# Kernel tuning notes

Hardware: AMD Instinct MI355X
Metric: run time of the kernel (lower is better)

The kernel has to match this reference:

```python
import jax, jax.numpy as jnp
import numpy as np

B, K, D, DS = 32, 64, 4, 4
H = 512            # hidden_dim
HH = H // 2        # hidden_hidden_dim = 256
NA = 2             # n_action


def _lin(k, out_d, in_d):
    kw, kb = jax.random.split(k)
    w = jax.random.normal(kw, (out_d, in_d), dtype=jnp.float32) * (in_d ** -0.5)
    b = jax.random.normal(kb, (out_d,), dtype=jnp.float32) * 0.01
    return w, b


def setup_inputs() -> dict:
    key = jax.random.key(0)
    ks = jax.random.split(key, 16)
    state = jax.random.normal(ks[0], (B, DS), dtype=jnp.float32)
    obs = jax.random.normal(ks[1], (B, D, K), dtype=jnp.float32)
    layer_w, layer_b = _lin(ks[2], H, DS)
    e1_w, e1_b = _lin(ks[3], H, 2 * D)
    e2_w, e2_b = _lin(ks[4], H, H)
    e3_w, e3_b = _lin(ks[5], H, H)
    ln_g = jnp.ones((H,), jnp.float32)
    ln_b = jnp.zeros((H,), jnp.float32)
    n1_w, n1_b = _lin(ks[6], H, D + H + DS)
    n2_w, n2_b = _lin(ks[7], HH, H)
    mu1_w, mu1_b = _lin(ks[8], 256, H + H)
    mu2_w, mu2_b = _lin(ks[9], 128, 256)
    mu3_w, mu3_b = _lin(ks[10], NA, 128)
    s1_w, s1_b = _lin(ks[11], 256, H + H)
    s2_w, s2_b = _lin(ks[12], 128, 256)
    s3_w, s3_b = _lin(ks[13], NA, 128)
    return dict(state=state, obs=obs, layer_w=layer_w, layer_b=layer_b,
                e1_w=e1_w, e1_b=e1_b, e2_w=e2_w, e2_b=e2_b, e3_w=e3_w, e3_b=e3_b,
                ln_g=ln_g, ln_b=ln_b, n1_w=n1_w, n1_b=n1_b, n2_w=n2_w, n2_b=n2_b,
                mu1_w=mu1_w, mu1_b=mu1_b, mu2_w=mu2_w, mu2_b=mu2_b, mu3_w=mu3_w, mu3_b=mu3_b,
                s1_w=s1_w, s1_b=s1_b, s2_w=s2_w, s2_b=s2_b, s3_w=s3_w, s3_b=s3_b)


def _dense(x, w, b):
    return x @ w.T + b


def reference(state, obs, layer_w, layer_b, e1_w, e1_b, e2_w, e2_b, e3_w, e3_b,
              ln_g, ln_b, n1_w, n1_b, n2_w, n2_b,
              mu1_w, mu1_b, mu2_w, mu2_b, mu3_w, mu3_b,
              s1_w, s1_b, s2_w, s2_b, s3_w, s3_b):
    # ---- InteractionNetwork ----
    o = jnp.transpose(obs, (0, 2, 1))                       # [B,K,D]
    mask = jnp.sum(jnp.abs(o), axis=2) != 0                 # [B,K] bool
    counts = jnp.clip(jnp.sum(mask, axis=1, keepdims=True).astype(o.dtype), 1e-6)  # [B,1]
    # all-pairs edge features [B,K,K,2D]
    obs_i = jnp.broadcast_to(o[:, :, None, :], (B, K, K, D))
    obs_j = jnp.broadcast_to(o[:, None, :, :], (B, K, K, D))
    edge_input = jnp.concatenate([obs_i, obs_j], axis=-1)
    h = jax.nn.relu(_dense(edge_input, e1_w, e1_b))
    h = jax.nn.relu(_dense(h, e2_w, e2_b))
    edge_output = jax.nn.relu(_dense(h, e3_w, e3_b))        # [B,K,K,H]
    edge_mask = (mask[:, :, None] & mask[:, None, :]).astype(o.dtype)  # [B,K,K]
    edge_output = edge_output * edge_mask[..., None]
    valid_counts = jnp.clip(jnp.sum(edge_mask, axis=2, keepdims=True), 1e-6)  # [B,K,1]
    agg = jnp.sum(edge_output, axis=2) / valid_counts       # [B,K,H]
    # LayerNorm (eps=1e-5, torch default)
    mu_ = jnp.mean(agg, axis=-1, keepdims=True)
    var_ = jnp.mean((agg - mu_) ** 2, axis=-1, keepdims=True)
    agg = (agg - mu_) * jax.lax.rsqrt(var_ + 1e-5) * ln_g + ln_b
    st_exp = jnp.broadcast_to(state[:, None, :], (B, K, DS))
    node_input = jnp.concatenate([o, agg, st_exp], axis=-1)  # [B,K,D+H+DS]
    node_output = _dense(jax.nn.relu(_dense(node_input, n1_w, n1_b)), n2_w, n2_b)  # [B,K,HH]
    m3 = mask[:, :, None]
    mean_pool = jnp.sum(jnp.where(m3, node_output, 0.0), axis=1) / counts  # [B,HH]
    max_pool = jnp.max(jnp.where(m3, node_output, -1e9), axis=1)           # [B,HH]
    obs_feat = jnp.concatenate([mean_pool, max_pool], axis=-1)             # [B,H]
    # ---- ActorNetwork head ----
    st_feat = jax.nn.relu(_dense(state, layer_w, layer_b))                 # [B,H]
    x = jnp.concatenate([st_feat, obs_feat], axis=1)                       # [B,2H]
    mu = _dense(jax.nn.relu(_dense(jax.nn.relu(_dense(x, mu1_w, mu1_b)), mu2_w, mu2_b)), mu3_w, mu3_b)
    std = jax.nn.softplus(_dense(jax.nn.relu(_dense(jax.nn.relu(_dense(x, s1_w, s1_b)), s2_w, s2_b)), s3_w, s3_b))
    std = jnp.clip(std + 0.001, 0.1, 2.0)
    return mu, std
```

## Files before the change

kernel.cpp:

```cpp
#include <hip/hip_runtime.h>
#include <hip/hip_fp16.h>

typedef _Float16 f16x8 __attribute__((ext_vector_type(8)));
typedef _Float16 f16x4 __attribute__((ext_vector_type(4)));
typedef float f32x4 __attribute__((ext_vector_type(4)));

#define NB 32
#define NK 64
#define ND 4
#define NH 512
#define NKP 544


__global__ void prep_obs_kernel(const float* __restrict__ obs,
                                const float* __restrict__ state,
                                float* __restrict__ o,
                                float* __restrict__ maskp,
                                float* __restrict__ cntp,
                                _Float16* __restrict__ nodein) {
  const int b = blockIdx.x;
  const int j = threadIdx.x;
  float o0 = obs[(b*4 + 0)*64 + j];
  float o1 = obs[(b*4 + 1)*64 + j];
  float o2 = obs[(b*4 + 2)*64 + j];
  float o3 = obs[(b*4 + 3)*64 + j];
  size_t bi = (size_t)b*64 + j;
  float* orow = o + bi*4;
  orow[0] = o0; orow[1] = o1; orow[2] = o2; orow[3] = o3;
  float s = fabsf(o0) + fabsf(o1) + fabsf(o2) + fabsf(o3);
  float m = (s != 0.0f) ? 1.0f : 0.0f;
  maskp[bi] = m;
  float c = m;
  #pragma unroll
  for (int off = 1; off < 64; off <<= 1) c += __shfl_xor(c, off);
  if (j == 0) cntp[b] = fmaxf(c, 1e-6f);
  _Float16* nrow = nodein + bi*NKP;
  nrow[0] = (_Float16)o0; nrow[1] = (_Float16)o1;
  nrow[2] = (_Float16)o2; nrow[3] = (_Float16)o3;
  nrow[516] = (_Float16)state[b*4 + 0];
  nrow[517] = (_Float16)state[b*4 + 1];
  nrow[518] = (_Float16)state[b*4 + 2];
  nrow[519] = (_Float16)state[b*4 + 3];
  for (int k2 = 520; k2 < 544; ++k2) nrow[k2] = (_Float16)0.0f;
}

__global__ __launch_bounds__(512) void prep_uv16(
    const float* __restrict__ o,
    const float* __restrict__ e1w,
    const float* __restrict__ e1b,
    _Float16* __restrict__ u16,
    _Float16* __restrict__ v16) {
  const int b = blockIdx.x;
  const int c = threadIdx.x;
  const float* wr = e1w + c*8;
  float4 wa = *(const float4*)wr;
  float4 wb = *(const float4*)(wr + 4);
  float bias = e1b[c];
  for (int j = 0; j < 64; ++j) {
    const int bi = b*64 + j;
    const float* orow = o + (size_t)bi*4;
    float4 ov = *(const float4*)orow;
    float u = wa.x*ov.x + wa.y*ov.y + wa.z*ov.z + wa.w*ov.w + bias;
    float v = wb.x*ov.x + wb.y*ov.y + wb.z*ov.z + wb.w*ov.w;
    u16[(size_t)bi*NH + c] = (_Float16)u;
    v16[(size_t)bi*NH + c] = (_Float16)v;
  }
}

__global__ void prep_w16_kernel(const float* __restrict__ e2w,
                                const float* __restrict__ e3w,
                                const float* __restrict__ n2w,
                                const float* __restrict__ n1w,
                                _Float16* __restrict__ w2h,
                                _Float16* __restrict__ w3h,
                                _Float16* __restrict__ n2wh,
                                _Float16* __restrict__ n1wh) {
  int idx = blockIdx.x * blockDim.x + threadIdx.x;
  const int A = 512*512, Bc = 512*512, C = 256*512, Dn = 512*544;
  if (idx < A) {
    w2h[idx] = (_Float16)e2w[idx];
  } else if (idx < A + Bc) {
    int q = idx - A; w3h[q] = (_Float16)e3w[q];
  } else if (idx < A + Bc + C) {
    int q = idx - A - Bc; n2wh[q] = (_Float16)n2w[q];
  } else if (idx < A + Bc + C + Dn) {
    int q = idx - A - Bc - C;
    int n = q / 544, k = q % 544;
    n1wh[q] = (k < 520) ? (_Float16)n1w[n*520 + k] : (_Float16)0.0f;
  }
}

__global__ void prep_stfeat_kernel(const float* __restrict__ state,
                                   const float* __restrict__ lw,
                                   const float* __restrict__ lb,
                                   float* __restrict__ xfeat) {
  const int b = blockIdx.x, c = threadIdx.x;
  const float* s = state + b*4;
  const float* wr = lw + c*4;
  float hv = wr[0]*s[0] + wr[1]*s[1] + wr[2]*s[2] + wr[3]*s[3] + lb[c];
  xfeat[b*1024 + c] = fmaxf(hv, 0.0f);
}


__device__ __forceinline__ void mlp_layer(const char* hb,
                                          const _Float16* __restrict__ wbase0,
                                          const float* __restrict__ biasp,
                                          int wcol, int lr, int lg,
                                          f32x4 acc[8][4]) {
  #pragma unroll
  for (int nt = 0; nt < 4; ++nt) {
    float bz = biasp[wcol + nt*16 + lr];
    #pragma unroll
    for (int mt = 0; mt < 8; ++mt) {
      acc[mt][nt][0] = bz; acc[mt][nt][1] = bz;
      acc[mt][nt][2] = bz; acc[mt][nt][3] = bz;
    }
  }
  const _Float16* bbase = wbase0 + (size_t)(wcol + lr)*NH + lg*8;
  f16x8 bfp[4];
  #pragma unroll
  for (int nt = 0; nt < 4; ++nt)
    bfp[nt] = *(const f16x8*)(bbase + nt*16*NH);

  f16x8 aflo[4];
  #pragma unroll
  for (int mt = 0; mt < 4; ++mt) {
    const int row = mt*16 + lr;
    aflo[mt] = *(const f16x8*)(hb + ((row*1024 + lg*16) ^ ((row & 7) << 4)));
  }

  for (int kk = 0; kk < 16; ++kk) {
    f16x8 bf[4];
    #pragma unroll
    for (int nt = 0; nt < 4; ++nt) bf[nt] = bfp[nt];
    if (kk < 15) {
      #pragma unroll
      for (int nt = 0; nt < 4; ++nt)
        bfp[nt] = *(const f16x8*)(bbase + nt*16*NH + (kk+1)*32);
    }
    f16x8 afhi[4];
    #pragma unroll
    for (int mt = 0; mt < 4; ++mt) {
      const int row = (mt + 4)*16 + lr;
      afhi[mt] = *(const f16x8*)(hb + ((row*1024 + kk*64 + lg*16) ^ ((row & 7) << 4)));
    }
    __builtin_amdgcn_s_setprio(1);
    #pragma unroll
    for (int mt = 0; mt < 4; ++mt)
      #pragma unroll
      for (int nt = 0; nt < 4; ++nt)
        acc[mt][nt] = __builtin_amdgcn_mfma_f32_16x16x32_f16(aflo[mt], bf[nt], acc[mt][nt], 0, 0, 0);
    __builtin_amdgcn_s_setprio(0);
    f16x8 aflon[4];
    if (kk < 15) {
      #pragma unroll
      for (int mt = 0; mt < 4; ++mt) {
        const int row = mt*16 + lr;
        aflon[mt] = *(const f16x8*)(hb + ((row*1024 + (kk+1)*64 + lg*16) ^ ((row & 7) << 4)));
      }
    }
    __builtin_amdgcn_s_setprio(1);
    #pragma unroll
    for (int mt = 0; mt < 4; ++mt)
      #pragma unroll
      for (int nt = 0; nt < 4; ++nt)
        acc[mt + 4][nt] = __builtin_amdgcn_mfma_f32_16x16x32_f16(afhi[mt], bf[nt], acc[mt + 4][nt], 0, 0, 0);
    __builtin_amdgcn_s_setprio(0);
    #pragma unroll
    for (int mt = 0; mt < 4; ++mt) aflo[mt] = aflon[mt];
  }
}

__global__ __launch_bounds__(512, 1) void edge_fused(
    const _Float16* __restrict__ u16, const _Float16* __restrict__ v16,
    const _Float16* __restrict__ w2h, const _Float16* __restrict__ w3h,
    const float* __restrict__ e2b, const float* __restrict__ e3b,
    const float* __restrict__ maskp, const float* __restrict__ cntp,
    const float* __restrict__ lng, const float* __restrict__ lnb,
    _Float16* __restrict__ nodein) {
  __shared__ __align__(16) char lds[131072];
  __shared__ float em_s[64];
  __shared__ float red_s[16];
  __shared__ float stat_s[2];

  const int t = threadIdx.x;
  const int bi0 = blockIdx.x * 2;
  const int b = bi0 >> 6;
  const int w = t >> 6, l = t & 63, lr = l & 15, lg = l >> 4;
  const int wcol = w * 64;

  if (t < 64) em_s[t] = maskp[(size_t)b*64 + t];

  {
    const int jrow = t >> 3;
    const int slot = t & 7;
    const _Float16* vrow = v16 + ((size_t)(b*64 + jrow))*NH;
    const _Float16* u0p  = u16 + (size_t)bi0*NH;
    const _Float16* u1p  = u16 + (size_t)(bi0 + 1)*NH;
    #pragma unroll
    for (int e = 0; e < 8; ++e) {
      const int kelem = e*64 + slot*8;
      f16x8 vv = *(const f16x8*)(vrow + kelem);
      f16x8 u0 = *(const f16x8*)(u0p + kelem);
      f16x8 u1 = *(const f16x8*)(u1p + kelem);
      f16x8 h0, h1;
      #pragma unroll
      for (int q = 0; q < 8; ++q) {
        _Float16 x0 = u0[q] + vv[q];
        _Float16 x1 = u1[q] + vv[q];
        h0[q] = x0 > (_Float16)0 ? x0 : (_Float16)0;
        h1[q] = x1 > (_Float16)0 ? x1 : (_Float16)0;
      }
      const int bc = kelem*2;
      const int r1 = 64 + jrow;
      *(f16x8*)(lds + ((jrow*1024 + bc) ^ ((jrow & 7) << 4))) = h0;
      *(f16x8*)(lds + ((r1*1024 + bc) ^ ((r1 & 7) << 4))) = h1;
    }
  }
  __syncthreads();

  f32x4 acc[8][4];

  mlp_layer(lds, w2h, e2b, wcol, lr, lg, acc);
  __syncthreads();

  #pragma unroll
  for (int mt = 0; mt < 8; ++mt)
    #pragma unroll
    for (int nt = 0; nt < 4; ++nt)
      #pragma unroll
      for (int r = 0; r < 4; ++r) {
        int row = mt*16 + lg*4 + r;
        int cc = wcol + nt*16 + lr;
        *(_Float16*)(lds + ((row*1024 + cc*2) ^ ((row & 7) << 4))) =
            (_Float16)fmaxf(acc[mt][nt][r], 0.0f);
      }
  __syncthreads();

  mlp_layer(lds, w3h, e3b, wcol, lr, lg, acc);

  float csum[2][4] = {{0.f,0.f,0.f,0.f},{0.f,0.f,0.f,0.f}};
  #pragma unroll
  for (int mt = 0; mt < 8; ++mt) {
    const int g = mt >> 2;
    float em0 = em_s[(mt&3)*16 + lg*4 + 0];
    float em1 = em_s[(mt&3)*16 + lg*4 + 1];
    float em2 = em_s[(mt&3)*16 + lg*4 + 2];
    float em3 = em_s[(mt&3)*16 + lg*4 + 3];
    #pragma unroll
    for (int nt = 0; nt < 4; ++nt) {
      csum[g][nt] += em0 * fmaxf(acc[mt][nt][0], 0.f)
                   + em1 * fmaxf(acc[mt][nt][1], 0.f)
                   + em2 * fmaxf(acc[mt][nt][2], 0.f)
                   + em3 * fmaxf(acc[mt][nt][3], 0.f);
    }
  }
  #pragma unroll
  for (int g = 0; g < 2; ++g)
    #pragma unroll
    for (int nt = 0; nt < 4; ++nt) {
      csum[g][nt] += __shfl_xor(csum[g][nt], 16);
      csum[g][nt] += __shfl_xor(csum[g][nt], 32);
    }
  float cnt = cntp[b];
  __syncthreads();
  float* aggs = (float*)lds;
  if (lg == 0) {
    #pragma unroll
    for (int g = 0; g < 2; ++g) {
      int big = bi0 + g;
      float sc = em_s[big & 63] / cnt;
      #pragma unroll
      for (int nt = 0; nt < 4; ++nt)
        aggs[g*512 + wcol + nt*16 + lr] = csum[g][nt] * sc;
    }
  }
  __syncthreads();

  for (int g = 0; g < 2; ++g) {
    float a = aggs[g*512 + t];
    float s1 = a, s2 = a * a;
    #pragma unroll
    for (int off = 1; off < 64; off <<= 1) {
      s1 += __shfl_xor(s1, off);
      s2 += __shfl_xor(s2, off);
    }
    if (l == 0) { red_s[w] = s1; red_s[8 + w] = s2; }
    __syncthreads();
    if (t == 0) {
      float S1 = 0.f, S2 = 0.f;
      #pragma unroll
      for (int q = 0; q < 8; ++q) { S1 += red_s[q]; S2 += red_s[8 + q]; }
      float mean = S1 * (1.0f/512.0f);
      float var = S2 * (1.0f/512.0f) - mean * mean;
      stat_s[0] = mean;
      stat_s[1] = rsqrtf(var + 1e-5f);
    }
    __syncthreads();
    float nrm = (a - stat_s[0]) * stat_s[1] * lng[t] + lnb[t];
    nodein[(size_t)(bi0 + g)*NKP + 4 + t] = (_Float16)nrm;
    __syncthreads();
  }
}


template <int RELU16>
__global__ __launch_bounds__(256) void node_gemm(
    const _Float16* __restrict__ A, const _Float16* __restrict__ Bw,
    const float* __restrict__ bias, void* __restrict__ outp,
    int Ka, int ldo) {
  const int t = threadIdx.x;
  const int w = t >> 6, l = t & 63, lr = l & 15, lg = l >> 4;
  const int m0 = blockIdx.x * 64;
  const int col = blockIdx.y * 64 + w*16 + lr;
  f32x4 acc[4];
  float bz = bias[col];
  #pragma unroll
  for (int mt = 0; mt < 4; ++mt) {
    acc[mt][0] = bz; acc[mt][1] = bz; acc[mt][2] = bz; acc[mt][3] = bz;
  }
  const _Float16* bptr = Bw + (size_t)col*Ka + lg*8;
  const _Float16* aptr = A + (size_t)(m0 + lr)*Ka + lg*8;
  const int nkk = Ka >> 5;
  for (int kk = 0; kk < nkk; ++kk) {
    f16x8 bf = *(const f16x8*)(bptr + kk*32);
    #pragma unroll
    for (int mt = 0; mt < 4; ++mt) {
      f16x8 af = *(const f16x8*)(aptr + ((size_t)mt*16)*Ka + kk*32);
      acc[mt] = __builtin_amdgcn_mfma_f32_16x16x32_f16(af, bf, acc[mt], 0, 0, 0);
    }
  }
  #pragma unroll
  for (int mt = 0; mt < 4; ++mt)
    #pragma unroll
    for (int r = 0; r < 4; ++r) {
      int row = m0 + mt*16 + lg*4 + r;
      float vv = acc[mt][r];
      if (RELU16)
        ((_Float16*)outp)[(size_t)row*ldo + col] = (_Float16)fmaxf(vv, 0.f);
      else
        ((float*)outp)[(size_t)row*ldo + col] = vv;
    }
}


__global__ __launch_bounds__(256) void pool_kernel(
    const float* __restrict__ nodeout, const float* __restrict__ maskp,
    const float* __restrict__ cntp, float* __restrict__ xfeat) {
  const int b = blockIdx.x;
  const int c = threadIdx.x;
  float sum = 0.f, mx = -1e9f;
  for (int i = 0; i < 64; ++i) {
    float m = maskp[b*64 + i];
    float v = nodeout[((size_t)(b*64 + i))*256 + c];
    sum += m * v;
    mx = fmaxf(mx, (m != 0.f) ? v : -1e9f);
  }
  xfeat[b*1024 + 512 + c] = sum / cntp[b];
  xfeat[b*1024 + 768 + c] = mx;
}

__global__ __launch_bounds__(256) void heads_g1(
    const float* __restrict__ xfeat,
    const float* __restrict__ mu1w, const float* __restrict__ s1w,
    float* __restrict__ part) {
  __shared__ __align__(16) float xs[256];
  const int b = blockIdx.x, h = blockIdx.y, ks = blockIdx.z;
  const int t = threadIdx.x;
  xs[t] = xfeat[b*1024 + ks*256 + t];
  __syncthreads();
  const float* wr = (h ? s1w : mu1w) + (size_t)t*1024 + ks*256;
  float a = 0.f;
  #pragma unroll 8
  for (int k = 0; k < 256; k += 4) {
    float4 ww = *(const float4*)(wr + k);
    float4 xx = *(const float4*)(xs + k);
    a += ww.x*xx.x + ww.y*xx.y + ww.z*xx.z + ww.w*xx.w;
  }
  part[(((size_t)(b*2 + h))*256 + t)*4 + ks] = a;
}

__global__ __launch_bounds__(256) void heads_g23(
    const float* __restrict__ part,
    const float* __restrict__ mu1b, const float* __restrict__ s1b,
    const float* __restrict__ mu2w, const float* __restrict__ mu2b,
    const float* __restrict__ s2w, const float* __restrict__ s2b,
    const float* __restrict__ mu3w, const float* __restrict__ mu3b,
    const float* __restrict__ s3w, const float* __restrict__ s3b,
    float* __restrict__ outp) {
  __shared__ __align__(16) float h1s[256];
  __shared__ __align__(16) float h2s[128];
  const int b = blockIdx.x, h = blockIdx.y;
  const int t = threadIdx.x;
  {
    float4 pp = *(const float4*)(part + (((size_t)(b*2 + h))*256 + t)*4);
    float a = pp.x + pp.y + pp.z + pp.w + (h ? s1b : mu1b)[t];
    h1s[t] = fmaxf(a, 0.f);
  }
  __syncthreads();
  {
    const int o = t >> 1, half = t & 1;
    const float* wr = (h ? s2w : mu2w) + (size_t)o*256 + half*128;
    const float* hp = h1s + half*128;
    float a = 0.f;
    #pragma unroll 8
    for (int k = 0; k < 128; k += 4) {
      float4 ww = *(const float4*)(wr + k);
      float4 hh = *(const float4*)(hp + k);
      a += ww.x*hh.x + ww.y*hh.y + ww.z*hh.z + ww.w*hh.w;
    }
    a += __shfl_xor(a, 1);
    if (half == 0) h2s[o] = fmaxf(a + (h ? s2b : mu2b)[o], 0.f);
  }
  __syncthreads();
  if (t < 64) {
    const int o = t >> 5, lane = t & 31;
    const float* wr = (h ? s3w : mu3w) + o*128 + lane*4;
    const float* hp = h2s + lane*4;
    float4 ww = *(const float4*)wr;
    float4 hh = *(const float4*)hp;
    float a = ww.x*hh.x + ww.y*hh.y + ww.z*hh.z + ww.w*hh.w;
    #pragma unroll
    for (int off = 1; off < 32; off <<= 1) a += __shfl_xor(a, off);
    if (lane == 0) {
      a += (h ? s3b : mu3b)[o];
      if (h == 0) {
        outp[b*2 + o] = a;
      } else {
        float spv = (a > 0.f) ? (a + log1pf(expf(-a))) : log1pf(expf(a));
        outp[64 + b*2 + o] = fminf(fmaxf(spv + 0.001f, 0.1f), 2.0f);
      }
    }
  }
}


extern "C" void kernel_launch(void* const* d_in, const int* in_sizes, int n_in,
                              void* d_out, int out_size, void* d_ws, size_t ws_size,
                              hipStream_t stream) {
  const float* state  = (const float*)d_in[0];
  const float* obs    = (const float*)d_in[1];
  const float* layerw = (const float*)d_in[2];
  const float* layerb = (const float*)d_in[3];
  const float* e1w    = (const float*)d_in[4];
  const float* e1b    = (const float*)d_in[5];
  const float* e2w    = (const float*)d_in[6];
  const float* e2b    = (const float*)d_in[7];
  const float* e3w    = (const float*)d_in[8];
  const float* e3b    = (const float*)d_in[9];
  const float* lng    = (const float*)d_in[10];
  const float* lnb    = (const float*)d_in[11];
  const float* n1w    = (const float*)d_in[12];
  const float* n1b    = (const float*)d_in[13];
  const float* n2w    = (const float*)d_in[14];
  const float* n2b    = (const float*)d_in[15];
  const float* mu1w   = (const float*)d_in[16];
  const float* mu1b   = (const float*)d_in[17];
  const float* mu2w   = (const float*)d_in[18];
  const float* mu2b   = (const float*)d_in[19];
  const float* mu3w   = (const float*)d_in[20];
  const float* mu3b   = (const float*)d_in[21];
  const float* s1w    = (const float*)d_in[22];
  const float* s1b    = (const float*)d_in[23];
  const float* s2w    = (const float*)d_in[24];
  const float* s2b    = (const float*)d_in[25];
  const float* s3w    = (const float*)d_in[26];
  const float* s3b    = (const float*)d_in[27];
  float* outp = (float*)d_out;

  char* p = (char*)d_ws;
  auto alloc = [&](size_t bytes) {
    char* r = p;
    p += (bytes + 255) & ~(size_t)255;
    return r;
  };
  float*    o       = (float*)alloc((size_t)2048*4*4);
  float*    maskp   = (float*)alloc((size_t)2048*4);
  float*    cntp    = (float*)alloc((size_t)32*4);
  _Float16* u16     = (_Float16*)alloc((size_t)2048*512*2);
  _Float16* v16     = (_Float16*)alloc((size_t)2048*512*2);
  _Float16* w2h     = (_Float16*)alloc((size_t)512*512*2);
  _Float16* w3h     = (_Float16*)alloc((size_t)512*512*2);
  _Float16* nodein  = (_Float16*)alloc((size_t)2048*544*2);
  _Float16* n1wh    = (_Float16*)alloc((size_t)512*544*2);
  _Float16* n2wh    = (_Float16*)alloc((size_t)256*512*2);
  _Float16* nodeh   = (_Float16*)alloc((size_t)2048*512*2);
  float*    nodeout = (float*)alloc((size_t)2048*256*4);
  float*    xfeat   = (float*)alloc((size_t)32*1024*4);
  float*    hpart   = (float*)alloc((size_t)32*2*256*4*4);

  prep_obs_kernel<<<32, 64, 0, stream>>>(obs, state, o, maskp, cntp, nodein);
  prep_uv16<<<32, 512, 0, stream>>>(o, e1w, e1b, u16, v16);
  prep_w16_kernel<<<3648, 256, 0, stream>>>(e2w, e3w, n2w, n1w, w2h, w3h, n2wh, n1wh);
  prep_stfeat_kernel<<<32, 512, 0, stream>>>(state, layerw, layerb, xfeat);

  edge_fused<<<1024, 512, 0, stream>>>(u16, v16, w2h, w3h, e2b, e3b,
                                       maskp, cntp, lng, lnb, nodein);

  node_gemm<1><<<dim3(32, 8), 256, 0, stream>>>(nodein, n1wh, n1b, (void*)nodeh, 544, 512);
  node_gemm<0><<<dim3(32, 4), 256, 0, stream>>>(nodeh, n2wh, n2b, (void*)nodeout, 512, 256);
  pool_kernel<<<32, 256, 0, stream>>>(nodeout, maskp, cntp, xfeat);
  heads_g1<<<dim3(32, 2, 4), 256, 0, stream>>>(xfeat, mu1w, s1w, hpart);
  heads_g23<<<dim3(32, 2), 256, 0, stream>>>(hpart, mu1b, s1b, mu2w, mu2b,
                                             s2w, s2b, mu3w, mu3b, s3w, s3b, outp);
}
```

Before: 230.1 us.

## Fuse prep kernels, fuse node MLP with pooling, deepen weight prefetch

Merges the observation prep, u/v edge projection and state-feature kernels into one launch that keeps obs in shared memory. Replaces the two node GEMMs and the pool kernel with a single per-batch kernel that keeps the hidden activations in LDS and does masked mean/max pooling in registers. This removes intermediate global buffers and launches. Separately, the edge MLP weight prefetch is deepened to two k-steps ahead. The fused node kernel runs only 32 blocks, so parallelism in the node stage drops compared with the earlier grid-split GEMMs.

```diff
diff --git a/kernel.cpp b/kernel.cpp
--- a/kernel.cpp
+++ b/kernel.cpp
@@ -12,58 +12,60 @@
 #define NKP 544
 
 
-__global__ void prep_obs_kernel(const float* __restrict__ obs,
-                                const float* __restrict__ state,
-                                float* __restrict__ o,
-                                float* __restrict__ maskp,
-                                float* __restrict__ cntp,
-                                _Float16* __restrict__ nodein) {
+__global__ __launch_bounds__(512) void prep_fused(
+    const float* __restrict__ obs, const float* __restrict__ state,
+    const float* __restrict__ e1w, const float* __restrict__ e1b,
+    const float* __restrict__ lw, const float* __restrict__ lb,
+    float* __restrict__ maskp, float* __restrict__ cntp,
+    _Float16* __restrict__ u16, _Float16* __restrict__ v16,
+    _Float16* __restrict__ nodein, float* __restrict__ xfeat) {
+  __shared__ __align__(16) float os[64][4];
+  __shared__ float st[4];
   const int b = blockIdx.x;
-  const int j = threadIdx.x;
-  float o0 = obs[(b*4 + 0)*64 + j];
-  float o1 = obs[(b*4 + 1)*64 + j];
-  float o2 = obs[(b*4 + 2)*64 + j];
-  float o3 = obs[(b*4 + 3)*64 + j];
-  size_t bi = (size_t)b*64 + j;
-  float* orow = o + bi*4;
-  orow[0] = o0; orow[1] = o1; orow[2] = o2; orow[3] = o3;
-  float s = fabsf(o0) + fabsf(o1) + fabsf(o2) + fabsf(o3);
-  float m = (s != 0.0f) ? 1.0f : 0.0f;
-  maskp[bi] = m;
-  float c = m;
-  #pragma unroll
-  for (int off = 1; off < 64; off <<= 1) c += __shfl_xor(c, off);
-  if (j == 0) cntp[b] = fmaxf(c, 1e-6f);
-  _Float16* nrow = nodein + bi*NKP;
-  nrow[0] = (_Float16)o0; nrow[1] = (_Float16)o1;
-  nrow[2] = (_Float16)o2; nrow[3] = (_Float16)o3;
-  nrow[516] = (_Float16)state[b*4 + 0];
-  nrow[517] = (_Float16)state[b*4 + 1];
-  nrow[518] = (_Float16)state[b*4 + 2];
-  nrow[519] = (_Float16)state[b*4 + 3];
-  for (int k2 = 520; k2 < 544; ++k2) nrow[k2] = (_Float16)0.0f;
-}
-
-__global__ __launch_bounds__(512) void prep_uv16(
-    const float* __restrict__ o,
-    const float* __restrict__ e1w,
-    const float* __restrict__ e1b,
-    _Float16* __restrict__ u16,
-    _Float16* __restrict__ v16) {
-  const int b = blockIdx.x;
-  const int c = threadIdx.x;
-  const float* wr = e1w + c*8;
-  float4 wa = *(const float4*)wr;
-  float4 wb = *(const float4*)(wr + 4);
-  float bias = e1b[c];
-  for (int j = 0; j < 64; ++j) {
-    const int bi = b*64 + j;
-    const float* orow = o + (size_t)bi*4;
-    float4 ov = *(const float4*)orow;
-    float u = wa.x*ov.x + wa.y*ov.y + wa.z*ov.z + wa.w*ov.w + bias;
-    float v = wb.x*ov.x + wb.y*ov.y + wb.z*ov.z + wb.w*ov.w;
-    u16[(size_t)bi*NH + c] = (_Float16)u;
-    v16[(size_t)bi*NH + c] = (_Float16)v;
+  const int t = threadIdx.x;
+  if (t < 4) st[t] = state[b*4 + t];
+  if (t < 64) {
+    float o0 = obs[(b*4 + 0)*64 + t];
+    float o1 = obs[(b*4 + 1)*64 + t];
+    float o2 = obs[(b*4 + 2)*64 + t];
+    float o3 = obs[(b*4 + 3)*64 + t];
+    os[t][0] = o0; os[t][1] = o1; os[t][2] = o2; os[t][3] = o3;
+    float s = fabsf(o0) + fabsf(o1) + fabsf(o2) + fabsf(o3);
+    float m = (s != 0.0f) ? 1.0f : 0.0f;
+    maskp[b*64 + t] = m;
+    float c = m;
+    #pragma unroll
+    for (int off = 1; off < 64; off <<= 1) c += __shfl_xor(c, off);
+    if (t == 0) cntp[b] = fmaxf(c, 1e-6f);
+    _Float16* nrow = nodein + (size_t)(b*64 + t)*NKP;
+    nrow[0] = (_Float16)o0; nrow[1] = (_Float16)o1;
+    nrow[2] = (_Float16)o2; nrow[3] = (_Float16)o3;
+    nrow[516] = (_Float16)state[b*4 + 0];
+    nrow[517] = (_Float16)state[b*4 + 1];
+    nrow[518] = (_Float16)state[b*4 + 2];
+    nrow[519] = (_Float16)state[b*4 + 3];
+    #pragma unroll
+    for (int k2 = 520; k2 < 544; ++k2) nrow[k2] = (_Float16)0.0f;
+  }
+  __syncthreads();
+  {
+    const float* wr = e1w + t*8;
+    float4 wa = *(const float4*)wr;
+    float4 wb = *(const float4*)(wr + 4);
+    float bias = e1b[t];
+    for (int j = 0; j < 64; ++j) {
+      float4 ov = *(const float4*)os[j];
+      float u = wa.x*ov.x + wa.y*ov.y + wa.z*ov.z + wa.w*ov.w + bias;
+      float v = wb.x*ov.x + wb.y*ov.y + wb.z*ov.z + wb.w*ov.w;
+      const size_t bi = (size_t)b*64 + j;
+      u16[bi*NH + t] = (_Float16)u;
+      v16[bi*NH + t] = (_Float16)v;
+    }
+  }
+  {
+    const float* wl = lw + t*4;
+    float hv = wl[0]*st[0] + wl[1]*st[1] + wl[2]*st[2] + wl[3]*st[3] + lb[t];
+    xfeat[b*1024 + t] = fmaxf(hv, 0.0f);
   }
 }
 
@@ -90,17 +92,6 @@
   }
 }
 
-__global__ void prep_stfeat_kernel(const float* __restrict__ state,
-                                   const float* __restrict__ lw,
-                                   const float* __restrict__ lb,
-                                   float* __restrict__ xfeat) {
-  const int b = blockIdx.x, c = threadIdx.x;
-  const float* s = state + b*4;
-  const float* wr = lw + c*4;
-  float hv = wr[0]*s[0] + wr[1]*s[1] + wr[2]*s[2] + wr[3]*s[3] + lb[c];
-  xfeat[b*1024 + c] = fmaxf(hv, 0.0f);
-}
-
 
 __device__ __forceinline__ void mlp_layer(const char* hb,
                                           const _Float16* __restrict__ wbase0,
@@ -117,10 +108,12 @@
     }
   }
   const _Float16* bbase = wbase0 + (size_t)(wcol + lr)*NH + lg*8;
-  f16x8 bfp[4];
+  f16x8 bfp0[4], bfp1[4];
   #pragma unroll
-  for (int nt = 0; nt < 4; ++nt)
-    bfp[nt] = *(const f16x8*)(bbase + nt*16*NH);
+  for (int nt = 0; nt < 4; ++nt) {
+    bfp0[nt] = *(const f16x8*)(bbase + nt*16*NH);
+    bfp1[nt] = *(const f16x8*)(bbase + nt*16*NH + 32);
+  }
 
   f16x8 aflo[4];
   #pragma unroll
@@ -132,11 +125,11 @@
   for (int kk = 0; kk < 16; ++kk) {
     f16x8 bf[4];
     #pragma unroll
-    for (int nt = 0; nt < 4; ++nt) bf[nt] = bfp[nt];
-    if (kk < 15) {
+    for (int nt = 0; nt < 4; ++nt) { bf[nt] = bfp0[nt]; bfp0[nt] = bfp1[nt]; }
+    if (kk < 14) {
       #pragma unroll
       for (int nt = 0; nt < 4; ++nt)
-        bfp[nt] = *(const f16x8*)(bbase + nt*16*NH + (kk+1)*32);
+        bfp1[nt] = *(const f16x8*)(bbase + nt*16*NH + (kk+2)*32);
     }
     f16x8 afhi[4];
     #pragma unroll
@@ -304,61 +297,125 @@
 }
 
 
-template <int RELU16>
-__global__ __launch_bounds__(256) void node_gemm(
-    const _Float16* __restrict__ A, const _Float16* __restrict__ Bw,
-    const float* __restrict__ bias, void* __restrict__ outp,
-    int Ka, int ldo) {
+__global__ __launch_bounds__(512, 1) void node_fused(
+    const _Float16* __restrict__ nodein,
+    const _Float16* __restrict__ n1wh, const float* __restrict__ n1b,
+    const _Float16* __restrict__ n2wh, const float* __restrict__ n2b,
+    const float* __restrict__ maskp, const float* __restrict__ cntp,
+    float* __restrict__ xfeat) {
+  __shared__ __align__(16) char lds[65536];
+  __shared__ float em_s[64];
+  const int b = blockIdx.x;
   const int t = threadIdx.x;
   const int w = t >> 6, l = t & 63, lr = l & 15, lg = l >> 4;
-  const int m0 = blockIdx.x * 64;
-  const int col = blockIdx.y * 64 + w*16 + lr;
-  f32x4 acc[4];
-  float bz = bias[col];
-  #pragma unroll
-  for (int mt = 0; mt < 4; ++mt) {
-    acc[mt][0] = bz; acc[mt][1] = bz; acc[mt][2] = bz; acc[mt][3] = bz;
-  }
-  const _Float16* bptr = Bw + (size_t)col*Ka + lg*8;
-  const _Float16* aptr = A + (size_t)(m0 + lr)*Ka + lg*8;
-  const int nkk = Ka >> 5;
-  for (int kk = 0; kk < nkk; ++kk) {
-    f16x8 bf = *(const f16x8*)(bptr + kk*32);
-    #pragma unroll
-    for (int mt = 0; mt < 4; ++mt) {
-      f16x8 af = *(const f16x8*)(aptr + ((size_t)mt*16)*Ka + kk*32);
-      acc[mt] = __builtin_amdgcn_mfma_f32_16x16x32_f16(af, bf, acc[mt], 0, 0, 0);
-    }
-  }
-  #pragma unroll
-  for (int mt = 0; mt < 4; ++mt)
-    #pragma unroll
-    for (int r = 0; r < 4; ++r) {
-      int row = m0 + mt*16 + lg*4 + r;
-      float vv = acc[mt][r];
-      if (RELU16)
-        ((_Float16*)outp)[(size_t)row*ldo + col] = (_Float16)fmaxf(vv, 0.f);
-      else
-        ((float*)outp)[(size_t)row*ldo + col] = vv;
-    }
-}
-
-
-__global__ __launch_bounds__(256) void pool_kernel(
-    const float* __restrict__ nodeout, const float* __restrict__ maskp,
-    const float* __restrict__ cntp, float* __restrict__ xfeat) {
-  const int b = blockIdx.x;
-  const int c = threadIdx.x;
-  float sum = 0.f, mx = -1e9f;
-  for (int i = 0; i < 64; ++i) {
-    float m = maskp[b*64 + i];
-    float v = nodeout[((size_t)(b*64 + i))*256 + c];
-    sum += m * v;
-    mx = fmaxf(mx, (m != 0.f) ? v : -1e9f);
-  }
-  xfeat[b*1024 + 512 + c] = sum / cntp[b];
-  xfeat[b*1024 + 768 + c] = mx;
-}
+
+  if (t < 64) em_s[t] = maskp[(size_t)b*64 + t];
+
+  {
+    const int wcol = w * 64;
+    f32x4 acc[4][4];
+    #pragma unroll
+    for (int nt = 0; nt < 4; ++nt) {
+      float bz = n1b[wcol + nt*16 + lr];
+      #pragma unroll
+      for (int mt = 0; mt < 4; ++mt) {
+        acc[mt][nt][0] = bz; acc[mt][nt][1] = bz;
+        acc[mt][nt][2] = bz; acc[mt][nt][3] = bz;
+      }
+    }
+    const _Float16* abase = nodein + ((size_t)(b*64 + lr))*NKP + lg*8;
+    const _Float16* bbase = n1wh + (size_t)(wcol + lr)*NKP + lg*8;
+    for (int kk = 0; kk < 17; ++kk) {
+      f16x8 af[4], bf[4];
+      #pragma unroll
+      for (int mt = 0; mt < 4; ++mt)
+        af[mt] = *(const f16x8*)(abase + ((size_t)mt*16)*NKP + kk*32);
+      #pragma unroll
+      for (int nt = 0; nt < 4; ++nt)
+        bf[nt] = *(const f16x8*)(bbase + ((size_t)nt*16)*NKP + kk*32);
+      #pragma unroll
+      for (int mt = 0; mt < 4; ++mt)
+        #pragma unroll
+        for (int nt = 0; nt < 4; ++nt)
+          acc[mt][nt] = __builtin_amdgcn_mfma_f32_16x16x32_f16(af[mt], bf[nt], acc[mt][nt], 0, 0, 0);
+    }
+    #pragma unroll
+    for (int mt = 0; mt < 4; ++mt)
+      #pragma unroll
+      for (int nt = 0; nt < 4; ++nt)
+        #pragma unroll
+        for (int r = 0; r < 4; ++r) {
+          int row = mt*16 + lg*4 + r;
+          int cc = wcol + nt*16 + lr;
+          *(_Float16*)(lds + ((row*1024 + cc*2) ^ ((row & 7) << 4))) =
+              (_Float16)fmaxf(acc[mt][nt][r], 0.0f);
+        }
+  }
+  __syncthreads();
+
+  {
+    const int wcol = w * 32;
+    f32x4 acc[4][2];
+    #pragma unroll
+    for (int nt = 0; nt < 2; ++nt) {
+      float bz = n2b[wcol + nt*16 + lr];
+      #pragma unroll
+      for (int mt = 0; mt < 4; ++mt) {
+        acc[mt][nt][0] = bz; acc[mt][nt][1] = bz;
+        acc[mt][nt][2] = bz; acc[mt][nt][3] = bz;
+      }
+    }
+    const _Float16* bbase = n2wh + (size_t)(wcol + lr)*NH + lg*8;
+    for (int kk = 0; kk < 16; ++kk) {
+      f16x8 bf[2];
+      #pragma unroll
+      for (int nt = 0; nt < 2; ++nt)
+        bf[nt] = *(const f16x8*)(bbase + nt*16*NH + kk*32);
+      f16x8 af[4];
+      #pragma unroll
+      for (int mt = 0; mt < 4; ++mt) {
+        const int row = mt*16 + lr;
+        af[mt] = *(const f16x8*)(lds + ((row*1024 + kk*64 + lg*16) ^ ((row & 7) << 4)));
+      }
+      #pragma unroll
+      for (int mt = 0; mt < 4; ++mt)
+        #pragma unroll
+        for (int nt = 0; nt < 2; ++nt)
+          acc[mt][nt] = __builtin_amdgcn_mfma_f32_16x16x32_f16(af[mt], bf[nt], acc[mt][nt], 0, 0, 0);
+    }
+    float sumv[2] = {0.f, 0.f};
+    float mxv[2] = {-1e9f, -1e9f};
+    #pragma unroll
+    for (int mt = 0; mt < 4; ++mt)
+      #pragma unroll
+      for (int r = 0; r < 4; ++r) {
+        float em = em_s[mt*16 + lg*4 + r];
+        #pragma unroll
+        for (int nt = 0; nt < 2; ++nt) {
+          float v = acc[mt][nt][r];
+          sumv[nt] += em * v;
+          mxv[nt] = fmaxf(mxv[nt], (em != 0.f) ? v : -1e9f);
+        }
+      }
+    #pragma unroll
+    for (int nt = 0; nt < 2; ++nt) {
+      sumv[nt] += __shfl_xor(sumv[nt], 16);
+      sumv[nt] += __shfl_xor(sumv[nt], 32);
+      mxv[nt] = fmaxf(mxv[nt], __shfl_xor(mxv[nt], 16));
+      mxv[nt] = fmaxf(mxv[nt], __shfl_xor(mxv[nt], 32));
+    }
+    float cnt = cntp[b];
+    if (lg == 0) {
+      #pragma unroll
+      for (int nt = 0; nt < 2; ++nt) {
+        int col = wcol + nt*16 + lr;
+        xfeat[b*1024 + 512 + col] = sumv[nt] / cnt;
+        xfeat[b*1024 + 768 + col] = mxv[nt];
+      }
+    }
+  }
+}
+
 
 __global__ __launch_bounds__(256) void heads_g1(
     const float* __restrict__ xfeat,
@@ -474,7 +531,6 @@
     p += (bytes + 255) & ~(size_t)255;
     return r;
   };
-  float*    o       = (float*)alloc((size_t)2048*4*4);
   float*    maskp   = (float*)alloc((size_t)2048*4);
   float*    cntp    = (float*)alloc((size_t)32*4);
   _Float16* u16     = (_Float16*)alloc((size_t)2048*512*2);
@@ -484,22 +540,18 @@
   _Float16* nodein  = (_Float16*)alloc((size_t)2048*544*2);
   _Float16* n1wh    = (_Float16*)alloc((size_t)512*544*2);
   _Float16* n2wh    = (_Float16*)alloc((size_t)256*512*2);
-  _Float16* nodeh   = (_Float16*)alloc((size_t)2048*512*2);
-  float*    nodeout = (float*)alloc((size_t)2048*256*4);
   float*    xfeat   = (float*)alloc((size_t)32*1024*4);
   float*    hpart   = (float*)alloc((size_t)32*2*256*4*4);
 
-  prep_obs_kernel<<<32, 64, 0, stream>>>(obs, state, o, maskp, cntp, nodein);
-  prep_uv16<<<32, 512, 0, stream>>>(o, e1w, e1b, u16, v16);
+  prep_fused<<<32, 512, 0, stream>>>(obs, state, e1w, e1b, layerw, layerb,
+                                     maskp, cntp, u16, v16, nodein, xfeat);
   prep_w16_kernel<<<3648, 256, 0, stream>>>(e2w, e3w, n2w, n1w, w2h, w3h, n2wh, n1wh);
-  prep_stfeat_kernel<<<32, 512, 0, stream>>>(state, layerw, layerb, xfeat);
 
   edge_fused<<<1024, 512, 0, stream>>>(u16, v16, w2h, w3h, e2b, e3b,
                                        maskp, cntp, lng, lnb, nodein);
 
-  node_gemm<1><<<dim3(32, 8), 256, 0, stream>>>(nodein, n1wh, n1b, (void*)nodeh, 544, 512);
-  node_gemm<0><<<dim3(32, 4), 256, 0, stream>>>(nodeh, n2wh, n2b, (void*)nodeout, 512, 256);
-  pool_kernel<<<32, 256, 0, stream>>>(nodeout, maskp, cntp, xfeat);
+  node_fused<<<32, 512, 0, stream>>>(nodein, n1wh, n1b, n2wh, n2b,
+                                     maskp, cntp, xfeat);
   heads_g1<<<dim3(32, 2, 4), 256, 0, stream>>>(xfeat, mu1w, s1w, hpart);
   heads_g23<<<dim3(32, 2), 256, 0, stream>>>(hpart, mu1b, s1b, mu2w, mu2b,
                                              s2w, s2b, mu3w, mu3b, s3w, s3b, outp);
```

New measurement: 310.4 us. 1.35x slower.
